# Kernel optimization log

Measured on AMD Instinct MI355X. Metric: run time of the kernel, lower is better.

## Reference

```python
import jax, jax.numpy as jnp
import numpy as np

EPS = 1e-12  # F.normalize default eps

def _l2norm(v, axis):
    n = jnp.sqrt(jnp.sum(v * v, axis=axis, keepdims=True))
    return v / jnp.maximum(n, EPS)

def setup_inputs() -> dict:
    key = jax.random.key(0)
    k1, k2, k3 = jax.random.split(key, 3)
    B, D, N, K = 32, 512, 2048, 64
    x = jax.random.normal(k1, (B, D, N), dtype=jnp.float32)
    # conv1d kernel_size=1, no bias -> weight [K, D]
    W = jax.random.normal(k2, (K, D), dtype=jnp.float32) * (1.0 / np.sqrt(D))
    # centers [D, K], xavier_uniform
    limit = np.sqrt(6.0 / (D + K))
    centers = jax.random.uniform(k3, (D, K), dtype=jnp.float32, minval=-limit, maxval=limit)
    return {"x": x, "W": W, "centers": centers}

def reference(x, W, centers):
    # x: [B, D, N], W: [K, D], centers: [D, K]
    scores = jnp.einsum('kd,bdn->bkn', W, x)          # [B, K, N]
    scores = jax.nn.softmax(scores, axis=1)            # softmax over K
    # sum_n scores[b,k,n] * (x[b,d,n] - centers[d,k])
    # = (scores @ x^T) - centers * sum_n scores   (linearity; avoids [B,D,K,N])
    agg = jnp.einsum('bkn,bdn->bdk', scores, x)        # [B, D, K]
    s_sum = jnp.sum(scores, axis=-1)                   # [B, K]
    desc = agg - centers[None, :, :] * s_sum[:, None, :]  # [B, D, K]
    desc = _l2norm(desc, axis=1)                       # intranorm over D
    B = x.shape[0]
    desc = desc.reshape(B, -1)                         # [B, D*K]
    desc = _l2norm(desc, axis=1)
    return desc
```

## Files before the change

kernel.cpp:

```cpp
#include <hip/hip_runtime.h>
#include <math.h>


typedef __attribute__((ext_vector_type(8))) short bf16x8;
typedef __attribute__((ext_vector_type(4))) float f32x4;

namespace {
constexpr int Bv = 32;
constexpr int Dv = 512;
constexpr int Nv = 2048;
constexpr int Kv = 64;
constexpr float EPSv = 1e-12f;
}

union Frag {
  uint4 q;
  bf16x8 v;
};

__device__ __forceinline__ unsigned pack2bf(float a, float b) {
  return (__float_as_uint(a) >> 16) | (__float_as_uint(b) & 0xFFFF0000u);
}
__device__ __forceinline__ float hi_f32(float a) {
  return __uint_as_float(__float_as_uint(a) & 0xFFFF0000u);
}
__device__ __forceinline__ void split8(const float4& a, const float4& b,
                                       uint4& h, uint4& l) {
  const float f[8] = {a.x, a.y, a.z, a.w, b.x, b.y, b.z, b.w};
  unsigned* hp = (unsigned*)&h;
  unsigned* lp = (unsigned*)&l;
#pragma unroll
  for (int j = 0; j < 4; ++j) {
    const float e = f[2 * j], o = f[2 * j + 1];
    hp[j] = pack2bf(e, o);
    lp[j] = pack2bf(e - hi_f32(e), o - hi_f32(o));
  }
}

__global__ __launch_bounds__(256) void k_prep(const float* __restrict__ W,
                                              float* __restrict__ out,
                                              float* __restrict__ aux,
                                              unsigned short* __restrict__ Whi,
                                              unsigned short* __restrict__ Wlo) {
  const int i = blockIdx.x * 256 + threadIdx.x;
  if (i < Bv * Dv * Kv) out[i] = 0.f;
  if (i < Kv * Dv) {
    const float w = W[i];
    Whi[i] = (unsigned short)(__float_as_uint(w) >> 16);
    Wlo[i] = (unsigned short)(__float_as_uint(w - hi_f32(w)) >> 16);
  }
  if (i < 2 * Bv * Kv) aux[i] = 0.f;
}

__global__ __launch_bounds__(256) void k_scores(const float* __restrict__ x,
                                                const unsigned short* __restrict__ Whi,
                                                const unsigned short* __restrict__ Wlo,
                                                float* __restrict__ p,
                                                float* __restrict__ s_sum) {
  const int b = blockIdx.y;
  const int n0 = blockIdx.x * 64;
  const int tid = threadIdx.x;
  const int lane = tid & 63;
  const int wv = tid >> 6;
  const int r = lane & 15;
  const int g = lane >> 4;

  __shared__ __align__(16) unsigned short wlds[2][2][64][40];
  __shared__ __align__(16) float xlds[2][32][68];
  float* plds = &xlds[0][0][0];

  const float* xb = x + (size_t)b * Dv * Nv;

  f32x4 acc[4];
#pragma unroll
  for (int mb = 0; mb < 4; ++mb) acc[mb] = (f32x4){0.f, 0.f, 0.f, 0.f};

  const int wk = tid >> 2;
  const int wdg = tid & 3;
  const int xd = tid >> 3;
  const int xng = tid & 7;

  uint4 rwh, rwl;
  float4 rxa, rxb;

#define GLOAD(s)                                                          \
  do {                                                                    \
    rwh = *(const uint4*)&Whi[wk * Dv + (s) * 32 + wdg * 8];              \
    rwl = *(const uint4*)&Wlo[wk * Dv + (s) * 32 + wdg * 8];              \
    const float* src = &xb[(size_t)((s) * 32 + xd) * Nv + n0 + xng * 8];  \
    rxa = *(const float4*)src;                                            \
    rxb = *(const float4*)(src + 4);                                      \
  } while (0)

#define LWRITE(buf)                                   \
  do {                                                \
    *(uint4*)&wlds[buf][0][wk][wdg * 8] = rwh;        \
    *(uint4*)&wlds[buf][1][wk][wdg * 8] = rwl;        \
    *(float4*)&xlds[buf][xd][xng * 8] = rxa;          \
    *(float4*)&xlds[buf][xd][xng * 8 + 4] = rxb;      \
  } while (0)

#define COMPUTE(buf)                                                          \
  do {                                                                        \
    float xf[8];                                                              \
    _Pragma("unroll") for (int j = 0; j < 8; ++j)                             \
        xf[j] = xlds[buf][g * 8 + j][wv * 16 + r];                            \
    Frag bh, bl;                                                              \
    _Pragma("unroll") for (int j = 0; j < 4; ++j) {                           \
      const float e = xf[2 * j], o = xf[2 * j + 1];                           \
      ((unsigned*)&bh.q)[j] = pack2bf(e, o);                                  \
      ((unsigned*)&bl.q)[j] = pack2bf(e - hi_f32(e), o - hi_f32(o));          \
    }                                                                         \
    _Pragma("unroll") for (int mb = 0; mb < 4; ++mb) {                        \
      Frag ah, al;                                                            \
      ah.q = *(const uint4*)&wlds[buf][0][mb * 16 + r][g * 8];                \
      al.q = *(const uint4*)&wlds[buf][1][mb * 16 + r][g * 8];                \
      acc[mb] = __builtin_amdgcn_mfma_f32_16x16x32_bf16(ah.v, bh.v, acc[mb], 0, 0, 0); \
      acc[mb] = __builtin_amdgcn_mfma_f32_16x16x32_bf16(ah.v, bl.v, acc[mb], 0, 0, 0); \
      acc[mb] = __builtin_amdgcn_mfma_f32_16x16x32_bf16(al.v, bh.v, acc[mb], 0, 0, 0); \
    }                                                                         \
  } while (0)

  GLOAD(0);
  LWRITE(0);
  __syncthreads();
  for (int s = 0; s < Dv / 32; ++s) {
    const int cur = s & 1;
    if (s + 1 < Dv / 32) GLOAD(s + 1);
    COMPUTE(cur);
    if (s + 1 < Dv / 32) LWRITE(cur ^ 1);
    __syncthreads();
  }
#undef GLOAD
#undef LWRITE
#undef COMPUTE

  float v[16];
#pragma unroll
  for (int mb = 0; mb < 4; ++mb)
#pragma unroll
    for (int q = 0; q < 4; ++q) v[mb * 4 + q] = acc[mb][q];

  float m = v[0];
#pragma unroll
  for (int i = 1; i < 16; ++i) m = fmaxf(m, v[i]);
  m = fmaxf(m, __shfl_xor(m, 16));
  m = fmaxf(m, __shfl_xor(m, 32));

  float sm = 0.f;
#pragma unroll
  for (int i = 0; i < 16; ++i) {
    v[i] = __expf(v[i] - m);
    sm += v[i];
  }
  sm += __shfl_xor(sm, 16);
  sm += __shfl_xor(sm, 32);
  const float rs = 1.f / sm;

  const int nl = wv * 16 + r;
#pragma unroll
  for (int mb = 0; mb < 4; ++mb)
#pragma unroll
    for (int q = 0; q < 4; ++q)
      plds[(mb * 16 + g * 4 + q) * 68 + nl] = v[mb * 4 + q] * rs;
  __syncthreads();

  const int pk = tid >> 2;
  const int png = tid & 3;
  const float4 p0 = *(const float4*)&plds[pk * 68 + png * 16];
  const float4 p1 = *(const float4*)&plds[pk * 68 + png * 16 + 4];
  const float4 p2 = *(const float4*)&plds[pk * 68 + png * 16 + 8];
  const float4 p3 = *(const float4*)&plds[pk * 68 + png * 16 + 12];
  const float part = (p0.x + p0.y + p0.z + p0.w) + (p1.x + p1.y + p1.z + p1.w) +
                     (p2.x + p2.y + p2.z + p2.w) + (p3.x + p3.y + p3.z + p3.w);
  atomicAdd(&s_sum[b * Kv + pk], part);
  float* dst = &p[((size_t)b * Kv + pk) * Nv + n0 + png * 16];
  *(float4*)dst = p0;
  *(float4*)(dst + 4) = p1;
  *(float4*)(dst + 8) = p2;
  *(float4*)(dst + 12) = p3;
}

__global__ __launch_bounds__(256) void k_agg(const float* __restrict__ x,
                                             const float* __restrict__ p,
                                             float* __restrict__ out) {
  const int d_base = blockIdx.x * 64;
  const int n_base = blockIdx.y * 512;
  const int b = blockIdx.z;
  const int tid = threadIdx.x;
  const int lane = tid & 63;
  const int wv = tid >> 6;
  const int wd = wv >> 1;
  const int wk = wv & 1;
  const int r = lane & 15;
  const int g = lane >> 4;

  __shared__ __align__(16) unsigned short xt[2][2][64][40];
  __shared__ __align__(16) unsigned short pt[2][2][64][40];

  const float* xb = x + (size_t)b * Dv * Nv;
  const float* pb = p + (size_t)b * Kv * Nv;

  f32x4 acc[2][2];
#pragma unroll
  for (int mb = 0; mb < 2; ++mb)
#pragma unroll
    for (int nb = 0; nb < 2; ++nb) acc[mb][nb] = (f32x4){0.f, 0.f, 0.f, 0.f};

  const int sr = tid >> 2;
  const int sg = tid & 3;

  float4 rx0, rx1, rp0, rp1;

#define GLOADA(s)                                                              \
  do {                                                                         \
    const float* sx = &xb[(size_t)(d_base + sr) * Nv + n_base + (s) * 32 + sg * 8]; \
    rx0 = *(const float4*)sx;                                                  \
    rx1 = *(const float4*)(sx + 4);                                            \
    const float* sp = &pb[(size_t)sr * Nv + n_base + (s) * 32 + sg * 8];       \
    rp0 = *(const float4*)sp;                                                  \
    rp1 = *(const float4*)(sp + 4);                                            \
  } while (0)

#define LWRITEA(buf)                                  \
  do {                                                \
    uint4 h, l;                                       \
    split8(rx0, rx1, h, l);                           \
    *(uint4*)&xt[buf][0][sr][sg * 8] = h;             \
    *(uint4*)&xt[buf][1][sr][sg * 8] = l;             \
    split8(rp0, rp1, h, l);                           \
    *(uint4*)&pt[buf][0][sr][sg * 8] = h;             \
    *(uint4*)&pt[buf][1][sr][sg * 8] = l;             \
  } while (0)

#define COMPUTEA(buf)                                                         \
  do {                                                                        \
    Frag xh[2], xl[2], ph[2], pl[2];                                          \
    _Pragma("unroll") for (int mb = 0; mb < 2; ++mb) {                        \
      xh[mb].q = *(const uint4*)&xt[buf][0][wd * 32 + mb * 16 + r][g * 8];    \
      xl[mb].q = *(const uint4*)&xt[buf][1][wd * 32 + mb * 16 + r][g * 8];    \
    }                                                                         \
    _Pragma("unroll") for (int nb = 0; nb < 2; ++nb) {                        \
      ph[nb].q = *(const uint4*)&pt[buf][0][wk * 32 + nb * 16 + r][g * 8];    \
      pl[nb].q = *(const uint4*)&pt[buf][1][wk * 32 + nb * 16 + r][g * 8];    \
    }                                                                         \
    _Pragma("unroll") for (int mb = 0; mb < 2; ++mb) {                        \
      _Pragma("unroll") for (int nb = 0; nb < 2; ++nb) {                      \
        acc[mb][nb] = __builtin_amdgcn_mfma_f32_16x16x32_bf16(xh[mb].v, ph[nb].v, acc[mb][nb], 0, 0, 0); \
        acc[mb][nb] = __builtin_amdgcn_mfma_f32_16x16x32_bf16(xh[mb].v, pl[nb].v, acc[mb][nb], 0, 0, 0); \
        acc[mb][nb] = __builtin_amdgcn_mfma_f32_16x16x32_bf16(xl[mb].v, ph[nb].v, acc[mb][nb], 0, 0, 0); \
      }                                                                       \
    }                                                                         \
  } while (0)

  GLOADA(0);
  LWRITEA(0);
  __syncthreads();
  const int STEPS = 512 / 32;
  for (int s = 0; s < STEPS; ++s) {
    const int cur = s & 1;
    if (s + 1 < STEPS) GLOADA(s + 1);
    COMPUTEA(cur);
    if (s + 1 < STEPS) LWRITEA(cur ^ 1);
    __syncthreads();
  }
#undef GLOADA
#undef LWRITEA
#undef COMPUTEA

#pragma unroll
  for (int mb = 0; mb < 2; ++mb) {
#pragma unroll
    for (int nb = 0; nb < 2; ++nb) {
#pragma unroll
      for (int q = 0; q < 4; ++q) {
        const int d = d_base + wd * 32 + mb * 16 + g * 4 + q;
        const int k = wk * 32 + nb * 16 + r;
        atomicAdd(&out[((size_t)b * Dv + d) * Kv + k], acc[mb][nb][q]);
      }
    }
  }
}

__global__ __launch_bounds__(256) void k_norm1(const float* __restrict__ out,
                                               const float* __restrict__ centers,
                                               const float* __restrict__ s_sum,
                                               float* __restrict__ colsq) {
  const int b = blockIdx.y;
  const int d0 = blockIdx.x * 64;
  const int k = threadIdx.x & 63;
  const int dq = threadIdx.x >> 6;

  __shared__ float red[4][64];

  const float sv = s_sum[b * Kv + k];
  float ssq = 0.f;
#pragma unroll
  for (int i = 0; i < 16; ++i) {
    const int d = d0 + dq * 16 + i;
    const float a = out[((size_t)b * Dv + d) * Kv + k];
    const float v = fmaf(-centers[d * Kv + k], sv, a);
    ssq = fmaf(v, v, ssq);
  }
  red[dq][k] = ssq;
  __syncthreads();
  if (threadIdx.x < 64) {
    const int kk = threadIdx.x;
    atomicAdd(&colsq[b * Kv + kk],
              red[0][kk] + red[1][kk] + red[2][kk] + red[3][kk]);
  }
}

__global__ __launch_bounds__(256) void k_norm2(float* __restrict__ out,
                                               const float* __restrict__ centers,
                                               const float* __restrict__ s_sum,
                                               const float* __restrict__ colsq) {
  const int b = blockIdx.y;
  const int d0 = blockIdx.x * 64;
  const int k = threadIdx.x & 63;
  const int dq = threadIdx.x >> 6;

  __shared__ float rns[64];
  __shared__ float red2[64];
  __shared__ float rtot_s;

  if (threadIdx.x < 64) {
    const float t = colsq[b * Kv + threadIdx.x];
    const float rn = 1.f / fmaxf(sqrtf(t), EPSv);
    rns[threadIdx.x] = rn;
    red2[threadIdx.x] = t * rn * rn;
  }
  __syncthreads();
  if (threadIdx.x == 0) {
    float t = 0.f;
#pragma unroll
    for (int kk = 0; kk < 64; ++kk) t += red2[kk];
    rtot_s = 1.f / fmaxf(sqrtf(t), EPSv);
  }
  __syncthreads();

  const float scale = rns[k] * rtot_s;
  const float sv = s_sum[b * Kv + k];
#pragma unroll
  for (int i = 0; i < 16; ++i) {
    const int d = d0 + dq * 16 + i;
    const size_t idx = ((size_t)b * Dv + d) * Kv + k;
    const float v = fmaf(-centers[d * Kv + k], sv, out[idx]);
    out[idx] = v * scale;
  }
}

extern "C" void kernel_launch(void* const* d_in, const int* in_sizes, int n_in,
                              void* d_out, int out_size, void* d_ws, size_t ws_size,
                              hipStream_t stream) {
  (void)in_sizes; (void)n_in; (void)out_size; (void)ws_size;
  const float* x = (const float*)d_in[0];
  const float* W = (const float*)d_in[1];
  const float* centers = (const float*)d_in[2];
  float* out = (float*)d_out;

  float* p = (float*)d_ws;
  float* s_sum = p + (size_t)Bv * Kv * Nv;
  float* colsq = s_sum + Bv * Kv;
  unsigned short* Whi = (unsigned short*)(colsq + Bv * Kv);
  unsigned short* Wlo = Whi + Kv * Dv;

  k_prep<<<dim3((Bv * Dv * Kv + 255) / 256), 256, 0, stream>>>(W, out, s_sum, Whi, Wlo);
  k_scores<<<dim3(Nv / 64, Bv), 256, 0, stream>>>(x, Whi, Wlo, p, s_sum);
  k_agg<<<dim3(Dv / 64, 4, Bv), 256, 0, stream>>>(x, p, out);
  k_norm1<<<dim3(Dv / 64, Bv), 256, 0, stream>>>(out, centers, s_sum, colsq);
  k_norm2<<<dim3(Dv / 64, Bv), 256, 0, stream>>>(out, centers, s_sum, colsq);
}
```

Baseline: 317.3 us.

## Drop split-N atomics in aggregation, use 512-thread blocks, deepen register prefetch

The aggregation kernel no longer splits N across four blocks with atomic adds. Each 512-thread block now covers the full N range for a 64-d tile with eight waves (2 over d, 4 over k) and writes results directly, so the zero-fill of the output in the prep kernel is removed. Both the scores and aggregation loops now prefetch two stages ahead using two register sets. This removes atomic traffic and the output memset, but cuts the aggregation grid fourfold (256 blocks), which may underfill the GPU and lengthen each block's serial loop.

```diff
diff --git a/kernel.cpp b/kernel.cpp
--- a/kernel.cpp
+++ b/kernel.cpp
@@ -24,26 +24,18 @@
 __device__ __forceinline__ float hi_f32(float a) {
   return __uint_as_float(__float_as_uint(a) & 0xFFFF0000u);
 }
-__device__ __forceinline__ void split8(const float4& a, const float4& b,
-                                       uint4& h, uint4& l) {
-  const float f[8] = {a.x, a.y, a.z, a.w, b.x, b.y, b.z, b.w};
-  unsigned* hp = (unsigned*)&h;
-  unsigned* lp = (unsigned*)&l;
-#pragma unroll
-  for (int j = 0; j < 4; ++j) {
-    const float e = f[2 * j], o = f[2 * j + 1];
-    hp[j] = pack2bf(e, o);
-    lp[j] = pack2bf(e - hi_f32(e), o - hi_f32(o));
-  }
+__device__ __forceinline__ void split4(const float4& f, uint2& h, uint2& l) {
+  h.x = pack2bf(f.x, f.y);
+  h.y = pack2bf(f.z, f.w);
+  l.x = pack2bf(f.x - hi_f32(f.x), f.y - hi_f32(f.y));
+  l.y = pack2bf(f.z - hi_f32(f.z), f.w - hi_f32(f.w));
 }
 
 __global__ __launch_bounds__(256) void k_prep(const float* __restrict__ W,
-                                              float* __restrict__ out,
                                               float* __restrict__ aux,
                                               unsigned short* __restrict__ Whi,
                                               unsigned short* __restrict__ Wlo) {
   const int i = blockIdx.x * 256 + threadIdx.x;
-  if (i < Bv * Dv * Kv) out[i] = 0.f;
   if (i < Kv * Dv) {
     const float w = W[i];
     Whi[i] = (unsigned short)(__float_as_uint(w) >> 16);
@@ -80,19 +72,19 @@
   const int xd = tid >> 3;
   const int xng = tid & 7;
 
-  uint4 rwh, rwl;
-  float4 rxa, rxb;
-
-#define GLOAD(s)                                                          \
+  uint4 rwhA, rwlA, rwhB, rwlB;
+  float4 rxaA, rxbA, rxaB, rxbB;
+
+#define GLOAD(S, rwh, rwl, rxa, rxb)                                      \
   do {                                                                    \
-    rwh = *(const uint4*)&Whi[wk * Dv + (s) * 32 + wdg * 8];              \
-    rwl = *(const uint4*)&Wlo[wk * Dv + (s) * 32 + wdg * 8];              \
-    const float* src = &xb[(size_t)((s) * 32 + xd) * Nv + n0 + xng * 8];  \
+    rwh = *(const uint4*)&Whi[wk * Dv + (S) * 32 + wdg * 8];              \
+    rwl = *(const uint4*)&Wlo[wk * Dv + (S) * 32 + wdg * 8];              \
+    const float* src = &xb[(size_t)((S) * 32 + xd) * Nv + n0 + xng * 8];  \
     rxa = *(const float4*)src;                                            \
     rxb = *(const float4*)(src + 4);                                      \
   } while (0)
 
-#define LWRITE(buf)                                   \
+#define LWRITE(buf, rwh, rwl, rxa, rxb)               \
   do {                                                \
     *(uint4*)&wlds[buf][0][wk][wdg * 8] = rwh;        \
     *(uint4*)&wlds[buf][1][wk][wdg * 8] = rwl;        \
@@ -121,14 +113,19 @@
     }                                                                         \
   } while (0)
 
-  GLOAD(0);
-  LWRITE(0);
-  __syncthreads();
-  for (int s = 0; s < Dv / 32; ++s) {
-    const int cur = s & 1;
-    if (s + 1 < Dv / 32) GLOAD(s + 1);
-    COMPUTE(cur);
-    if (s + 1 < Dv / 32) LWRITE(cur ^ 1);
+  GLOAD(0, rwhA, rwlA, rxaA, rxbA);
+  GLOAD(1, rwhB, rwlB, rxaB, rxbB);
+  LWRITE(0, rwhA, rwlA, rxaA, rxbA);
+  __syncthreads();
+
+  for (int s = 0; s < 16; s += 2) {
+    if (s + 2 < 16) GLOAD(s + 2, rwhA, rwlA, rxaA, rxbA);
+    COMPUTE(0);
+    LWRITE(1, rwhB, rwlB, rxaB, rxbB);
+    __syncthreads();
+    if (s + 3 < 16) GLOAD(s + 3, rwhB, rwlB, rxaB, rxbB);
+    COMPUTE(1);
+    if (s + 2 < 16) LWRITE(0, rwhA, rwlA, rxaA, rxbA);
     __syncthreads();
   }
 #undef GLOAD
@@ -181,17 +178,16 @@
   *(float4*)(dst + 12) = p3;
 }
 
-__global__ __launch_bounds__(256) void k_agg(const float* __restrict__ x,
+__global__ __launch_bounds__(512) void k_agg(const float* __restrict__ x,
                                              const float* __restrict__ p,
                                              float* __restrict__ out) {
   const int d_base = blockIdx.x * 64;
-  const int n_base = blockIdx.y * 512;
-  const int b = blockIdx.z;
+  const int b = blockIdx.y;
   const int tid = threadIdx.x;
   const int lane = tid & 63;
   const int wv = tid >> 6;
-  const int wd = wv >> 1;
-  const int wk = wv & 1;
+  const int wd = wv >> 2;
+  const int wk = wv & 3;
   const int r = lane & 15;
   const int g = lane >> 4;
 
@@ -201,67 +197,62 @@
   const float* xb = x + (size_t)b * Dv * Nv;
   const float* pb = p + (size_t)b * Kv * Nv;
 
-  f32x4 acc[2][2];
-#pragma unroll
-  for (int mb = 0; mb < 2; ++mb)
-#pragma unroll
-    for (int nb = 0; nb < 2; ++nb) acc[mb][nb] = (f32x4){0.f, 0.f, 0.f, 0.f};
-
-  const int sr = tid >> 2;
-  const int sg = tid & 3;
-
-  float4 rx0, rx1, rp0, rp1;
-
-#define GLOADA(s)                                                              \
-  do {                                                                         \
-    const float* sx = &xb[(size_t)(d_base + sr) * Nv + n_base + (s) * 32 + sg * 8]; \
-    rx0 = *(const float4*)sx;                                                  \
-    rx1 = *(const float4*)(sx + 4);                                            \
-    const float* sp = &pb[(size_t)sr * Nv + n_base + (s) * 32 + sg * 8];       \
-    rp0 = *(const float4*)sp;                                                  \
-    rp1 = *(const float4*)(sp + 4);                                            \
-  } while (0)
-
-#define LWRITEA(buf)                                  \
+  f32x4 acc[2];
+#pragma unroll
+  for (int mb = 0; mb < 2; ++mb) acc[mb] = (f32x4){0.f, 0.f, 0.f, 0.f};
+
+  const int sr = tid >> 3;
+  const int sg = tid & 7;
+
+  float4 rxA, rpA, rxB, rpB;
+
+#define GLOADA(S, rx, rp)                                                 \
+  do {                                                                    \
+    rx = *(const float4*)&xb[(size_t)(d_base + sr) * Nv + (S) * 32 + sg * 4]; \
+    rp = *(const float4*)&pb[(size_t)sr * Nv + (S) * 32 + sg * 4];        \
+  } while (0)
+
+#define LWRITEA(buf, rx, rp)                          \
   do {                                                \
-    uint4 h, l;                                       \
-    split8(rx0, rx1, h, l);                           \
-    *(uint4*)&xt[buf][0][sr][sg * 8] = h;             \
-    *(uint4*)&xt[buf][1][sr][sg * 8] = l;             \
-    split8(rp0, rp1, h, l);                           \
-    *(uint4*)&pt[buf][0][sr][sg * 8] = h;             \
-    *(uint4*)&pt[buf][1][sr][sg * 8] = l;             \
+    uint2 h, l;                                       \
+    split4(rx, h, l);                                 \
+    *(uint2*)&xt[buf][0][sr][sg * 4] = h;             \
+    *(uint2*)&xt[buf][1][sr][sg * 4] = l;             \
+    split4(rp, h, l);                                 \
+    *(uint2*)&pt[buf][0][sr][sg * 4] = h;             \
+    *(uint2*)&pt[buf][1][sr][sg * 4] = l;             \
   } while (0)
 
 #define COMPUTEA(buf)                                                         \
   do {                                                                        \
-    Frag xh[2], xl[2], ph[2], pl[2];                                          \
+    Frag xh[2], xl[2], ph, pl;                                                \
     _Pragma("unroll") for (int mb = 0; mb < 2; ++mb) {                        \
       xh[mb].q = *(const uint4*)&xt[buf][0][wd * 32 + mb * 16 + r][g * 8];    \
       xl[mb].q = *(const uint4*)&xt[buf][1][wd * 32 + mb * 16 + r][g * 8];    \
     }                                                                         \
-    _Pragma("unroll") for (int nb = 0; nb < 2; ++nb) {                        \
-      ph[nb].q = *(const uint4*)&pt[buf][0][wk * 32 + nb * 16 + r][g * 8];    \
-      pl[nb].q = *(const uint4*)&pt[buf][1][wk * 32 + nb * 16 + r][g * 8];    \
+    ph.q = *(const uint4*)&pt[buf][0][wk * 16 + r][g * 8];                    \
+    pl.q = *(const uint4*)&pt[buf][1][wk * 16 + r][g * 8];                    \
+    _Pragma("unroll") for (int mb = 0; mb < 2; ++mb) {                        \
+      acc[mb] = __builtin_amdgcn_mfma_f32_16x16x32_bf16(xh[mb].v, ph.v, acc[mb], 0, 0, 0); \
+      acc[mb] = __builtin_amdgcn_mfma_f32_16x16x32_bf16(xh[mb].v, pl.v, acc[mb], 0, 0, 0); \
+      acc[mb] = __builtin_amdgcn_mfma_f32_16x16x32_bf16(xl[mb].v, ph.v, acc[mb], 0, 0, 0); \
     }                                                                         \
-    _Pragma("unroll") for (int mb = 0; mb < 2; ++mb) {                        \
-      _Pragma("unroll") for (int nb = 0; nb < 2; ++nb) {                      \
-        acc[mb][nb] = __builtin_amdgcn_mfma_f32_16x16x32_bf16(xh[mb].v, ph[nb].v, acc[mb][nb], 0, 0, 0); \
-        acc[mb][nb] = __builtin_amdgcn_mfma_f32_16x16x32_bf16(xh[mb].v, pl[nb].v, acc[mb][nb], 0, 0, 0); \
-        acc[mb][nb] = __builtin_amdgcn_mfma_f32_16x16x32_bf16(xl[mb].v, ph[nb].v, acc[mb][nb], 0, 0, 0); \
-      }                                                                       \
-    }                                                                         \
-  } while (0)
-
-  GLOADA(0);
-  LWRITEA(0);
-  __syncthreads();
-  const int STEPS = 512 / 32;
-  for (int s = 0; s < STEPS; ++s) {
-    const int cur = s & 1;
-    if (s + 1 < STEPS) GLOADA(s + 1);
-    COMPUTEA(cur);
-    if (s + 1 < STEPS) LWRITEA(cur ^ 1);
+  } while (0)
+
+  GLOADA(0, rxA, rpA);
+  GLOADA(1, rxB, rpB);
+  LWRITEA(0, rxA, rpA);
+  __syncthreads();
+
+  const int STEPS = Nv / 32;
+  for (int s = 0; s < STEPS; s += 2) {
+    if (s + 2 < STEPS) GLOADA(s + 2, rxA, rpA);
+    COMPUTEA(0);
+    LWRITEA(1, rxB, rpB);
+    __syncthreads();
+    if (s + 3 < STEPS) GLOADA(s + 3, rxB, rpB);
+    COMPUTEA(1);
+    if (s + 2 < STEPS) LWRITEA(0, rxA, rpA);
     __syncthreads();
   }
 #undef GLOADA
@@ -271,13 +262,10 @@
 #pragma unroll
   for (int mb = 0; mb < 2; ++mb) {
 #pragma unroll
-    for (int nb = 0; nb < 2; ++nb) {
-#pragma unroll
-      for (int q = 0; q < 4; ++q) {
-        const int d = d_base + wd * 32 + mb * 16 + g * 4 + q;
-        const int k = wk * 32 + nb * 16 + r;
-        atomicAdd(&out[((size_t)b * Dv + d) * Kv + k], acc[mb][nb][q]);
-      }
+    for (int q = 0; q < 4; ++q) {
+      const int d = d_base + wd * 32 + mb * 16 + g * 4 + q;
+      const int k = wk * 16 + r;
+      out[((size_t)b * Dv + d) * Kv + k] = acc[mb][q];
     }
   }
 }
@@ -365,9 +353,9 @@
   unsigned short* Whi = (unsigned short*)(colsq + Bv * Kv);
   unsigned short* Wlo = Whi + Kv * Dv;
 
-  k_prep<<<dim3((Bv * Dv * Kv + 255) / 256), 256, 0, stream>>>(W, out, s_sum, Whi, Wlo);
+  k_prep<<<dim3((Kv * Dv + 255) / 256), 256, 0, stream>>>(W, s_sum, Whi, Wlo);
   k_scores<<<dim3(Nv / 64, Bv), 256, 0, stream>>>(x, Whi, Wlo, p, s_sum);
-  k_agg<<<dim3(Dv / 64, 4, Bv), 256, 0, stream>>>(x, p, out);
+  k_agg<<<dim3(Dv / 64, Bv), 512, 0, stream>>>(x, p, out);
   k_norm1<<<dim3(Dv / 64, Bv), 256, 0, stream>>>(out, centers, s_sum, colsq);
   k_norm2<<<dim3(Dv / 64, Bv), 256, 0, stream>>>(out, centers, s_sum, colsq);
 }
```

Result: no change. 322.7 us (+1.7%).
